# Kernel tuning notes

Hardware: AMD Instinct MI355X
Metric: run time of the kernel (lower is better)

Reference implementation:

```python
import jax, jax.numpy as jnp
import numpy as np

N_HEADS = 16

def setup_inputs() -> dict:
    key = jax.random.key(0)
    k1, k2 = jax.random.split(key)
    B, S, H = 4, 2048, 1024
    hidden_states = jax.random.normal(k1, (B, S, H), dtype=jnp.float32)
    # F.linear weight: [out_features, in_features]; init std per module
    std = 0.02 / np.sqrt(2.0 * 24 * H)
    queries_weight = jax.random.normal(k2, (H, H), dtype=jnp.float32) * std
    return {"hidden_states": hidden_states, "queries_weight": queries_weight}


def reference(hidden_states, queries_weight):
    B, S, H = hidden_states.shape
    hd = H // N_HEADS
    # F.linear: x @ W^T
    q = hidden_states @ queries_weight.T
    qh = q.reshape(B, S, N_HEADS, hd)          # [B,S,h,d]
    xh = hidden_states.reshape(B, S, N_HEADS, hd)
    # pre_attn = Q K^T (no softmax), then attn @ V with K=V=x heads
    pre_attn = jnp.einsum('bqhd,bkhd->bhqk', qh, xh)   # [B,h,S,S]
    attn = jnp.einsum('bhqk,bkhd->bqhd', pre_attn, xh) # [B,S,h,d]
    return attn.reshape(B, S, H)
```

## Files before the change

kernel.cpp:

```cpp
#include <hip/hip_runtime.h>
#include <hip/hip_bf16.h>


typedef __bf16 bf16x8 __attribute__((ext_vector_type(8)));
typedef float f32x4 __attribute__((ext_vector_type(4)));

typedef __attribute__((address_space(3))) unsigned int lds_u32;
typedef const __attribute__((address_space(1))) unsigned int glb_u32;

__device__ __forceinline__ void gld_lds16(const void* g, void* l) {
    __builtin_amdgcn_global_load_lds((glb_u32*)g, (lds_u32*)l, 16, 0, 0);
}

__device__ __forceinline__ unsigned short f2bf(float f) {
    unsigned int u = __float_as_uint(f);
    u += 0x7FFFu + ((u >> 16) & 1u);
    return (unsigned short)(u >> 16);
}

#define XT_S 136

__global__ __launch_bounds__(256) void gx_partial(
        const float* __restrict__ x, const float* __restrict__ W,
        unsigned short* __restrict__ xb, unsigned short* __restrict__ Wb,
        float* __restrict__ Gp) {
    __shared__ __align__(16) unsigned short xt[64 * XT_S];
    const int tid = threadIdx.x;
    const int chunk = blockIdx.x;
    const int bh = blockIdx.y;
    const int fb = bh * 8 + chunk;
    const int b = bh >> 4, h = bh & 15;
    const int wave = tid >> 6, lane = tid & 63;
    const int lm = lane & 15, quad = lane >> 4;

    {
        size_t base = (size_t)fb * 2048 + (size_t)tid * 8;
        float4 v0 = *(const float4*)&W[base];
        float4 v1 = *(const float4*)&W[base + 4];
        ushort4 o0 = {f2bf(v0.x), f2bf(v0.y), f2bf(v0.z), f2bf(v0.w)};
        ushort4 o1 = {f2bf(v1.x), f2bf(v1.y), f2bf(v1.z), f2bf(v1.w)};
        *(ushort4*)&Wb[base] = o0;
        *(ushort4*)&Wb[base + 4] = o1;
    }

    f32x4 acc[4] = {};
    for (int half = 0; half < 2; ++half) {
        const size_t gbase =
            ((size_t)(b * 2048 + chunk * 256 + half * 128)) * 1024 + h * 64;
        __syncthreads();
        #pragma unroll
        for (int i = 0; i < 8; ++i) {
            int idx = tid + 256 * i;
            int s = idx >> 4;
            int c = (idx & 15) * 4;
            float4 v = *(const float4*)&x[gbase + (size_t)s * 1024 + c];
            ushort4 o = {f2bf(v.x), f2bf(v.y), f2bf(v.z), f2bf(v.w)};
            *(ushort4*)&xb[gbase + (size_t)s * 1024 + c] = o;
            xt[(c + 0) * XT_S + s] = o.x;
            xt[(c + 1) * XT_S + s] = o.y;
            xt[(c + 2) * XT_S + s] = o.z;
            xt[(c + 3) * XT_S + s] = o.w;
        }
        __syncthreads();
        #pragma unroll
        for (int k = 0; k < 4; ++k) {
            bf16x8 af = *(const bf16x8*)&xt[(wave * 16 + lm) * XT_S + k * 32 + quad * 8];
            #pragma unroll
            for (int ni = 0; ni < 4; ++ni) {
                bf16x8 bg = *(const bf16x8*)&xt[(ni * 16 + lm) * XT_S + k * 32 + quad * 8];
                acc[ni] = __builtin_amdgcn_mfma_f32_16x16x32_bf16(af, bg, acc[ni], 0, 0, 0);
            }
        }
    }
    float* gp = Gp + ((size_t)(chunk * 64 + bh)) * 4096;
    #pragma unroll
    for (int ni = 0; ni < 4; ++ni)
        #pragma unroll
        for (int r = 0; r < 4; ++r)
            gp[(wave * 16 + quad * 4 + r) * 64 + ni * 16 + lm] = acc[ni][r];
}

__global__ __launch_bounds__(256) void g_reduce(
        const float* __restrict__ Gp, unsigned short* __restrict__ Gb) {
    const int bh = blockIdx.x;
    const int e0 = blockIdx.y * 1024 + threadIdx.x * 4;
    float4 s = {0.f, 0.f, 0.f, 0.f};
    #pragma unroll
    for (int c = 0; c < 8; ++c) {
        float4 v = *(const float4*)&Gp[((size_t)(c * 64 + bh)) * 4096 + e0];
        s.x += v.x; s.y += v.y; s.z += v.z; s.w += v.w;
    }
    ushort4 o;
    o.x = f2bf(s.x); o.y = f2bf(s.y); o.z = f2bf(s.z); o.w = f2bf(s.w);
    *(ushort4*)&Gb[(size_t)bh * 4096 + e0] = o;
}

__global__ __launch_bounds__(256, 2) void gemm_qout(
        const unsigned short* __restrict__ xb, const unsigned short* __restrict__ Wb,
        const unsigned short* __restrict__ Gb, float* __restrict__ out) {
    __shared__ __align__(16) unsigned short smem[26624];
    unsigned short* lA = smem;
    unsigned short* lB = smem + 8192;
    unsigned short* Qt = smem;
    unsigned short* G2 = smem + 17408;
    const int tid = threadIdx.x;
    const int m0 = blockIdx.x * 128;
    const int n0 = blockIdx.y * 128;
    const int b  = blockIdx.x >> 4;
    const int h0 = blockIdx.y * 2;
    const int lane = tid & 63, wave = tid >> 6;
    const int wr = (wave >> 1) * 64, wc = (wave & 1) * 64;
    const int lm = lane & 15, quad = lane >> 4;
    const int srow = wave * 32 + (lane >> 3);
    const int scol = (((lane & 7) ^ ((lane >> 3) & 7))) * 8;

    #pragma unroll
    for (int i = 0; i < 4; ++i) {
        int idx = tid + 256 * i;
        int hh = idx >> 9;
        int rr = (idx >> 3) & 63;
        int cc = (idx & 7) * 8;
        *(uint4*)&G2[hh * 4608 + rr * 72 + cc] =
            *(const uint4*)&Gb[((size_t)(b * 16 + h0 + hh)) * 4096 + rr * 64 + cc];
    }

    f32x4 acc[4][4] = {};
    for (int kt = 0; kt < 1024; kt += 64) {
        const unsigned short* ga = &xb[(size_t)(m0 + srow) * 1024 + kt + scol];
        const unsigned short* gb = &Wb[(size_t)(n0 + srow) * 1024 + kt + scol];
        #pragma unroll
        for (int i = 0; i < 4; ++i) {
            gld_lds16(ga + (size_t)i * 8 * 1024, &lA[(wave * 32 + i * 8) * 64]);
            gld_lds16(gb + (size_t)i * 8 * 1024, &lB[(wave * 32 + i * 8) * 64]);
        }
        __syncthreads();
        #pragma unroll
        for (int kk = 0; kk < 2; ++kk) {
            bf16x8 af[4], bg[4];
            #pragma unroll
            for (int mi = 0; mi < 4; ++mi) {
                int ra = wr + mi * 16 + lm;
                int jb = (kk * 4 + quad) ^ (ra & 7);
                af[mi] = *(const bf16x8*)&lA[ra * 64 + jb * 8];
            }
            #pragma unroll
            for (int ni = 0; ni < 4; ++ni) {
                int rb = wc + ni * 16 + lm;
                int jb = (kk * 4 + quad) ^ (rb & 7);
                bg[ni] = *(const bf16x8*)&lB[rb * 64 + jb * 8];
            }
            #pragma unroll
            for (int mi = 0; mi < 4; ++mi)
                #pragma unroll
                for (int ni = 0; ni < 4; ++ni)
                    acc[mi][ni] = __builtin_amdgcn_mfma_f32_16x16x32_bf16(
                        af[mi], bg[ni], acc[mi][ni], 0, 0, 0);
        }
        __syncthreads();
    }
    #pragma unroll
    for (int mi = 0; mi < 4; ++mi)
        #pragma unroll
        for (int ni = 0; ni < 4; ++ni)
            #pragma unroll
            for (int r = 0; r < 4; ++r)
                Qt[(wr + mi * 16 + quad * 4 + r) * 136 + wc + ni * 16 + lm] =
                    f2bf(acc[mi][ni][r]);
    #pragma unroll
    for (int mi = 0; mi < 4; ++mi)
        #pragma unroll
        for (int ni = 0; ni < 4; ++ni)
            acc[mi][ni] = (f32x4){0.f, 0.f, 0.f, 0.f};
    const int hh = wave & 1;
    #pragma unroll
    for (int kk = 0; kk < 2; ++kk) {
        bf16x8 af[4], bg[4];
        #pragma unroll
        for (int mi = 0; mi < 4; ++mi)
            af[mi] = *(const bf16x8*)&Qt[(wr + mi * 16 + lm) * 136 + wc + kk * 32 + quad * 8];
        #pragma unroll
        for (int ni = 0; ni < 4; ++ni)
            bg[ni] = *(const bf16x8*)&G2[hh * 4608 + (ni * 16 + lm) * 72 + kk * 32 + quad * 8];
        #pragma unroll
        for (int mi = 0; mi < 4; ++mi)
            #pragma unroll
            for (int ni = 0; ni < 4; ++ni)
                acc[mi][ni] = __builtin_amdgcn_mfma_f32_16x16x32_bf16(
                    af[mi], bg[ni], acc[mi][ni], 0, 0, 0);
    }
    #pragma unroll
    for (int mi = 0; mi < 4; ++mi)
        #pragma unroll
        for (int ni = 0; ni < 4; ++ni)
            #pragma unroll
            for (int r = 0; r < 4; ++r)
                out[(size_t)(m0 + wr + mi * 16 + quad * 4 + r) * 1024
                    + n0 + wc + ni * 16 + lm] = acc[mi][ni][r];
}

extern "C" void kernel_launch(void* const* d_in, const int* in_sizes, int n_in,
                              void* d_out, int out_size, void* d_ws, size_t ws_size,
                              hipStream_t stream) {
    const float* x = (const float*)d_in[0];
    const float* W = (const float*)d_in[1];
    float* out = (float*)d_out;
    char* ws = (char*)d_ws;
    unsigned short* xb = (unsigned short*)(ws);
    unsigned short* Wb = (unsigned short*)(ws + 16777216);
    float*          Gp = (float*)        (ws + 18874368);
    unsigned short* Gb = (unsigned short*)(ws + 27262976);

    gx_partial<<<dim3(8, 64), 256, 0, stream>>>(x, W, xb, Wb, Gp);
    g_reduce<<<dim3(64, 4), 256, 0, stream>>>(Gp, Gb);
    gemm_qout<<<dim3(64, 8), 256, 0, stream>>>(xb, Wb, Gb, out);
}
```

Baseline: 113.6 us.

## Fuse Gram reduction into gx_partial via a grid-wide atomic barrier

```diff
diff --git a/kernel.cpp b/kernel.cpp
--- a/kernel.cpp
+++ b/kernel.cpp
@@ -20,10 +20,11 @@
 
 #define XT_S 136
 
-__global__ __launch_bounds__(256) void gx_partial(
+__global__ __launch_bounds__(256, 2) void gx_partial(
         const float* __restrict__ x, const float* __restrict__ W,
         unsigned short* __restrict__ xb, unsigned short* __restrict__ Wb,
-        float* __restrict__ Gp) {
+        float* __restrict__ Gp, unsigned short* __restrict__ Gb,
+        unsigned* __restrict__ ctr) {
     __shared__ __align__(16) unsigned short xt[64 * XT_S];
     const int tid = threadIdx.x;
     const int chunk = blockIdx.x;
@@ -78,21 +79,28 @@
         #pragma unroll
         for (int r = 0; r < 4; ++r)
             gp[(wave * 16 + quad * 4 + r) * 64 + ni * 16 + lm] = acc[ni][r];
-}
-
-__global__ __launch_bounds__(256) void g_reduce(
-        const float* __restrict__ Gp, unsigned short* __restrict__ Gb) {
-    const int bh = blockIdx.x;
-    const int e0 = blockIdx.y * 1024 + threadIdx.x * 4;
-    float4 s = {0.f, 0.f, 0.f, 0.f};
-    #pragma unroll
-    for (int c = 0; c < 8; ++c) {
-        float4 v = *(const float4*)&Gp[((size_t)(c * 64 + bh)) * 4096 + e0];
-        s.x += v.x; s.y += v.y; s.z += v.z; s.w += v.w;
-    }
-    ushort4 o;
-    o.x = f2bf(s.x); o.y = f2bf(s.y); o.z = f2bf(s.z); o.w = f2bf(s.w);
-    *(ushort4*)&Gb[(size_t)bh * 4096 + e0] = o;
+
+    __threadfence();
+    __syncthreads();
+    if (tid == 0) {
+        atomicAdd(ctr, 1u);
+        int guard = 1 << 22;
+        while (atomicAdd(ctr, 0u) < 512u && --guard) ;
+        __threadfence();
+    }
+    __syncthreads();
+
+    {
+        int e0 = chunk * 512 + tid * 2;
+        float2 s = {0.f, 0.f};
+        #pragma unroll
+        for (int c = 0; c < 8; ++c) {
+            float2 v = *(const float2*)&Gp[((size_t)(c * 64 + bh)) * 4096 + e0];
+            s.x += v.x; s.y += v.y;
+        }
+        ushort2 o = {f2bf(s.x), f2bf(s.y)};
+        *(ushort2*)&Gb[(size_t)bh * 4096 + e0] = o;
+    }
 }
 
 __global__ __launch_bounds__(256, 2) void gemm_qout(
@@ -209,8 +217,9 @@
     unsigned short* Wb = (unsigned short*)(ws + 16777216);
     float*          Gp = (float*)        (ws + 18874368);
     unsigned short* Gb = (unsigned short*)(ws + 27262976);
-
-    gx_partial<<<dim3(8, 64), 256, 0, stream>>>(x, W, xb, Wb, Gp);
-    g_reduce<<<dim3(64, 4), 256, 0, stream>>>(Gp, Gb);
+    unsigned*       ctr = (unsigned*)    (ws + 27787264);
+
+    hipMemsetAsync(ctr, 0, 64, stream);
+    gx_partial<<<dim3(8, 64), 256, 0, stream>>>(x, W, xb, Wb, Gp, Gb, ctr);
     gemm_qout<<<dim3(64, 8), 256, 0, stream>>>(xb, Wb, Gb, out);
 }
```

Measured after the change: 220.1 us. +93.7%, slower.
